# Optimization experiments

Measured on AMD Instinct MI355X. Metric: run time of the kernel, lower is better.

## Reference

```python
import jax, jax.numpy as jnp
import numpy as np

B, N, F, T = 16, 1024, 32, 12
K, FC, FT, TS, D = 3, 64, 64, 1, 16
THETA_THR = 0.6
LN_EPS = 1e-5


def setup_inputs() -> dict:
    key = jax.random.key(0)
    ks = jax.random.split(key, 20)
    r = lambda i, shape, s=0.1: jax.random.normal(ks[i], shape, dtype=jnp.float32) * s
    return dict(
        x=jax.random.normal(ks[0], (B, N, F, T), dtype=jnp.float32),
        node_embeddings=r(1, (N, D), 1.0),
        W1=r(2, (T,)), W2=r(3, (F, T)), W3=r(4, (F,)),
        bs=r(5, (1, N, N)), Vs=r(6, (N, N)),
        U1=r(7, (N,)), U2=r(8, (F, N)), U3=r(9, (F,)),
        be=r(10, (1, T, T)), Ve=r(11, (T, T)),
        Theta=r(12, (K, F, FC)),
        tc_v=r(13, (FT, FC, 1, 3)), tc_g=jnp.ones((FT,), jnp.float32), tc_b=r(14, (FT,)),
        rc_w=r(15, (FT, F, 1, 1)), rc_b=r(16, (FT,)),
        ln_w=jnp.ones((FT,), jnp.float32), ln_b=jnp.zeros((FT,), jnp.float32),
    )


def _forward(x, node_embeddings, W1, W2, W3, bs, Vs, U1, U2, U3, be, Ve,
             Theta, tc_v, tc_g, tc_b, rc_w, rc_b, ln_w, ln_b):
    b, n, f, t = x.shape
    k_order = Theta.shape[0]

    # --- temporal attention: E (B,T,T) ---
    lhs = jnp.einsum('bnft,n->btf', x, U1) @ U2                # (B,T,N)
    rhs = jnp.einsum('f,bnft->bnt', U3, x)                     # (B,N,T)
    prod = jnp.einsum('btn,bnu->btu', lhs, rhs)                # (B,T,T)
    E = jnp.einsum('ts,bsu->btu', Ve, jax.nn.sigmoid(prod + be))
    E = jax.nn.softmax(E, axis=1)

    # x_TAt = reshape(B, N*F, T) @ E  (equivalent einsum over t)
    x_TAt = jnp.einsum('bnft,btu->bnfu', x, E)                 # (B,N,F,T)

    # --- sparse spatial attention on x_TAt: (B,N,N) ---
    l2 = jnp.einsum('bnft,t->bnf', x_TAt, W1) @ W2             # (B,N,T)
    r2 = jnp.einsum('f,bnft->btn', W3, x_TAt)                  # (B,T,N)
    prod2 = jnp.einsum('bnt,btm->bnm', l2, r2)                 # (B,N,N)
    S = jnp.einsum('nm,bmk->bnk', Vs, jax.nn.sigmoid(prod2 + bs))
    Sn = jax.nn.softmax(S, axis=1)
    thr = jnp.mean(Sn) / THETA_THR
    spat = jnp.where(Sn < thr, jnp.zeros_like(Sn), Sn)         # Sparse_S_normalized

    # --- K-order adaptive graph conv with attention mask ---
    sup = jax.nn.softmax(jax.nn.relu(node_embeddings @ node_embeddings.T), axis=1)
    polys = [jnp.eye(n, dtype=x.dtype), sup]
    for k in range(2, k_order):
        polys.append(2.0 * sup @ polys[-1] - polys[-2])
    out = jnp.zeros((b, t, n, Theta.shape[2]), x.dtype)
    for k in range(k_order):
        A = polys[k][None] * spat                              # (B,N,N)
        h = jnp.einsum('bnm,bnft->btmf', A, x)                 # A^T @ x per timestep
        out = out + jnp.einsum('btmf,fo->btmo', h, Theta[k])
    gcn = jax.nn.relu(out)                                     # (B,T,N,FC)

    # --- time conv (weight-normed 1x3) + residual 1x1 conv ---
    vnorm = jnp.sqrt(jnp.sum(tc_v * tc_v, axis=(1, 2, 3), keepdims=True))
    w = tc_g[:, None, None, None] * tc_v / vnorm
    inp = gcn.transpose(0, 3, 2, 1)                            # (B,FC,N,T)
    tco = jax.lax.conv_general_dilated(
        inp, w, (1, TS), ((0, 0), (1, 1)),
        dimension_numbers=('NCHW', 'OIHW', 'NCHW')) + tc_b[None, :, None, None]
    res = jax.lax.conv_general_dilated(
        x.transpose(0, 2, 1, 3), rc_w, (1, TS), ((0, 0), (0, 0)),
        dimension_numbers=('NCHW', 'OIHW', 'NCHW')) + rc_b[None, :, None, None]

    # --- layernorm over channel dim ---
    y = (res + tco).transpose(0, 3, 2, 1)                      # (B,T,N,FT)
    mu = jnp.mean(y, axis=-1, keepdims=True)
    var = jnp.var(y, axis=-1, keepdims=True)
    y = (y - mu) / jnp.sqrt(var + LN_EPS) * ln_w + ln_b
    x_res = y.transpose(0, 2, 3, 1)                            # (B,N,FT,T)
    return x_res, spat


def reference(x, node_embeddings, W1, W2, W3, bs, Vs, U1, U2, U3, be, Ve,
              Theta, tc_v, tc_g, tc_b, rc_w, rc_b, ln_w, ln_b):
    return _forward(x, node_embeddings, W1, W2, W3, bs, Vs, U1, U2, U3, be, Ve,
                    Theta, tc_v, tc_g, tc_b, rc_w, rc_b, ln_w, ln_b)
```

## Files before the change

kernel.cpp:

```cpp
#include <hip/hip_runtime.h>
#include <math.h>

#define NB 16
#define NN 1024
#define NF 32
#define NT 12
#define NFC 64
#define NFT 64

typedef __attribute__((ext_vector_type(8))) short bf16x8;
typedef __attribute__((ext_vector_type(4))) float f32x4;

__device__ inline unsigned short cvt_bf(float f) {
    unsigned int u = __float_as_uint(f);
    u += 0x7fff + ((u >> 16) & 1);
    return (unsigned short)(u >> 16);
}
__device__ inline float bf2f(unsigned short u) {
    return __uint_as_float(((unsigned int)u) << 16);
}
__device__ inline void gll16(const short* g, short* l) {
    __builtin_amdgcn_global_load_lds((const __attribute__((address_space(1))) void*)g,
                                     (__attribute__((address_space(3))) void*)l, 16, 0, 0);
}

__global__ __launch_bounds__(384) void k_pre(const float* __restrict__ x,
                                             const float* __restrict__ U1,
                                             const float* __restrict__ U3,
                                             const float* __restrict__ W3,
                                             float* __restrict__ lhs_pre,
                                             float* __restrict__ rhs,
                                             float* __restrict__ rr3,
                                             unsigned short* __restrict__ Xrow)
{
    __shared__ float xs[8 * 384];
    int b = blockIdx.x, ch = blockIdx.y, tid = threadIdx.x;
    float acc = 0.f;
    for (int c8 = 0; c8 < 8; c8++) {
        int n0 = ch * 64 + c8 * 8;
        size_t r0 = (size_t)b * NN + n0;
        __syncthreads();
        for (int i = 0; i < 8; i++) xs[i * 384 + tid] = x[(r0 + i) * 384 + tid];
        __syncthreads();
        for (int i = 0; i < 8; i++) acc += xs[i * 384 + tid] * U1[n0 + i];
        for (int idx = tid; idx < 1536; idx += 384) {
            int row = idx / 192, jj = (idx - row * 192) * 2;
            unsigned int w = (unsigned int)cvt_bf(xs[row * 384 + jj])
                           | ((unsigned int)cvt_bf(xs[row * 384 + jj + 1]) << 16);
            *(unsigned int*)(Xrow + (r0 + row) * 384 + jj) = w;
        }
        if (tid < 192) {
            int half = tid / 96;
            int r = tid - half * 96;
            int i = r / 12, t = r - i * 12;
            const float* wv = half ? W3 : U3;
            float s = 0.f;
            for (int f = 0; f < 32; f++) s += wv[f] * xs[i * 384 + f * 12 + t];
            float* outp = half ? rr3 : rhs;
            outp[(r0 + i) * 12 + t] = s;
        }
    }
    int f = tid / 12, t = tid - f * 12;
    atomicAdd(&lhs_pre[b * 384 + t * 32 + f], acc);
}

__global__ __launch_bounds__(256) void k_lhs(const float* __restrict__ lhs_pre,
                                             const float* __restrict__ U2,
                                             float* __restrict__ lhs)
{
    int bt = blockIdx.x;
    int tid = threadIdx.x;
    __shared__ float lp[32];
    if (tid < 32) lp[tid] = lhs_pre[bt * 32 + tid];
    __syncthreads();
    for (int q = 0; q < 4; q++) {
        int n = q * 256 + tid;
        float a = 0.f;
        for (int f = 0; f < 32; f++) a += lp[f] * U2[f * NN + n];
        lhs[(size_t)bt * NN + n] = a;
    }
}

__global__ __launch_bounds__(64) void k_prod(const float* __restrict__ lhs,
                                             const float* __restrict__ rhs,
                                             float* __restrict__ prod)
{
    int blk = blockIdx.x;
    int b = blk / 144, r = blk - b * 144;
    int s = r / 12, u = r - s * 12;
    int tid = threadIdx.x;
    float p = 0.f;
    for (int n = tid; n < NN; n += 64)
        p += lhs[((size_t)b * 12 + s) * NN + n] * rhs[((size_t)b * NN + n) * 12 + u];
    for (int o = 32; o > 0; o >>= 1) p += __shfl_xor(p, o);
    if (tid == 0) prod[blk] = p;
}

__global__ __launch_bounds__(192) void k_E(const float* __restrict__ prod,
                                           const float* __restrict__ be,
                                           const float* __restrict__ Ve,
                                           const float* __restrict__ W1,
                                           float* __restrict__ E,
                                           float* __restrict__ EW1)
{
    int b = blockIdx.x, tid = threadIdx.x;
    __shared__ float ssig[144], sE[144], mx[12], sm[12];
    if (tid < 144) ssig[tid] = 1.f / (1.f + expf(-(prod[b * 144 + tid] + be[tid])));
    __syncthreads();
    if (tid < 144) {
        int t = tid / 12, u = tid - t * 12;
        float a = 0.f;
        for (int s2 = 0; s2 < 12; s2++) a += Ve[t * 12 + s2] * ssig[s2 * 12 + u];
        sE[tid] = a;
    }
    __syncthreads();
    if (tid < 12) {
        float m = -1e30f;
        for (int t = 0; t < 12; t++) m = fmaxf(m, sE[t * 12 + tid]);
        float s = 0.f;
        for (int t = 0; t < 12; t++) s += expf(sE[t * 12 + tid] - m);
        mx[tid] = m; sm[tid] = s;
    }
    __syncthreads();
    float val = 0.f;
    if (tid < 144) {
        int u = tid % 12;
        val = expf(sE[tid] - mx[u]) / sm[u];
        E[b * 144 + tid] = val;
    }
    __syncthreads();
    if (tid < 144) sE[tid] = val;
    __syncthreads();
    if (tid < 12) {
        float a = 0.f;
        for (int u = 0; u < 12; u++) a += sE[tid * 12 + u] * W1[u];
        EW1[b * 12 + tid] = a;
    }
}

__global__ __launch_bounds__(384) void k_l2r2x(const unsigned short* __restrict__ Xrow,
                                               const float* __restrict__ rr3,
                                               const float* __restrict__ E,
                                               const float* __restrict__ EW1,
                                               const float* __restrict__ W2,
                                               float* __restrict__ l2,
                                               float* __restrict__ r2)
{
    __shared__ float xs[8 * 384];
    __shared__ float Es[144], ew[12], rrs[96], lp[8][32];
    int b = blockIdx.y, tid = threadIdx.x;
    int n0 = blockIdx.x * 8;
    size_t r0 = (size_t)b * NN + n0;
    if (tid < 144) Es[tid] = E[b * 144 + tid];
    if (tid < 12) ew[tid] = EW1[b * 12 + tid];
    if (tid < 96) rrs[tid] = rr3[(r0 + tid / 12) * 12 + (tid % 12)];
    const unsigned int* Xr = (const unsigned int*)(Xrow + r0 * 384);
    for (int i2 = tid; i2 < 1536; i2 += 384) {
        unsigned int w = Xr[i2];
        xs[2 * i2]     = bf2f((unsigned short)(w & 0xffff));
        xs[2 * i2 + 1] = bf2f((unsigned short)(w >> 16));
    }
    __syncthreads();
    if (tid < 256) {
        int i = tid >> 5, f = tid & 31;
        float a = 0.f;
#pragma unroll
        for (int t = 0; t < 12; t++) a += xs[i * 384 + f * 12 + t] * ew[t];
        lp[i][f] = a;
    }
    __syncthreads();
    if (tid < 96) {
        int i = tid / 12, u = tid - i * 12;
        float a = 0.f;
        for (int f = 0; f < 32; f++) a += lp[i][f] * W2[f * 12 + u];
        l2[(r0 + i) * 12 + u] = a;
        float rv = 0.f;
#pragma unroll
        for (int t = 0; t < 12; t++) rv += rrs[i * 12 + t] * Es[t * 12 + u];
        r2[((size_t)b * 12 + u) * NN + n0 + i] = rv;
    }
}

__global__ __launch_bounds__(256) void k_xt(const unsigned short* __restrict__ Xrow,
                                            unsigned short* __restrict__ Xt)
{
    __shared__ unsigned short tl[64][66];
    int b = blockIdx.z;
    int n0 = blockIdx.y * 64, j0 = blockIdx.x * 64;
    int tid = threadIdx.x;
    int c = tid & 63, r0 = tid >> 6;
    for (int i = 0; i < 16; i++) {
        int r = r0 + i * 4;
        tl[r][c] = Xrow[((size_t)b * NN + n0 + r) * 384 + j0 + c];
    }
    __syncthreads();
    int c2 = tid & 31, r4 = tid >> 5;
    unsigned short* ob = Xt + ((size_t)b * 384 + j0) * NN + n0;
    for (int i = 0; i < 8; i++) {
        int jr = r4 + i * 8;
        unsigned int v0 = (unsigned int)tl[2 * c2][jr] | ((unsigned int)tl[2 * c2 + 1][jr] << 16);
        *(unsigned int*)(ob + (size_t)jr * NN + 2 * c2) = v0;
    }
}

__global__ __launch_bounds__(256) void k_Ptile(const float* __restrict__ l2,
                                               const float* __restrict__ r2,
                                               const float* __restrict__ bsin,
                                               unsigned short* __restrict__ Pt)
{
    __shared__ float l2s[64][13];
    __shared__ float r2s[12][64];
    __shared__ float bsS[64][65];
    int k0 = blockIdx.x * 64, m0 = blockIdx.y * 64, b = blockIdx.z;
    int tid = threadIdx.x;
    for (int i = tid; i < 768; i += 256) {
        int r = i / 12, t = i - r * 12;
        l2s[r][t] = l2[((size_t)b * NN + m0 + r) * 12 + t];
    }
    for (int i = tid; i < 768; i += 256) {
        int t = i >> 6, k = i & 63;
        r2s[t][k] = r2[((size_t)b * 12 + t) * NN + k0 + k];
    }
    for (int i = tid; i < 4096; i += 256) {
        int r = i >> 6, c = i & 63;
        bsS[r][c] = bsin[(size_t)(m0 + r) * NN + k0 + c];
    }
    __syncthreads();
    int m = tid & 63, kg = tid >> 6;
    float lv[12];
#pragma unroll
    for (int t = 0; t < 12; t++) lv[t] = l2s[m][t];
#pragma unroll
    for (int s = 0; s < 16; s++) {
        int kl = kg * 16 + s;
        float p = bsS[m][kl];
#pragma unroll
        for (int t = 0; t < 12; t++) p += lv[t] * r2s[t][kl];
        float sg = 1.f / (1.f + expf(-p));
        Pt[((size_t)b * NN + k0 + kl) * NN + m0 + m] = cvt_bf(sg);
    }
}

__global__ __launch_bounds__(256) void k_cvt(const float* __restrict__ s,
                                             unsigned short* __restrict__ d)
{
    size_t i = ((size_t)blockIdx.x * 256 + threadIdx.x) * 4;
    float4 v = *(const float4*)(s + i);
    unsigned int p0 = (unsigned int)cvt_bf(v.x) | ((unsigned int)cvt_bf(v.y) << 16);
    unsigned int p1 = (unsigned int)cvt_bf(v.z) | ((unsigned int)cvt_bf(v.w) << 16);
    *(unsigned int*)(d + i) = p0;
    *(unsigned int*)(d + i + 2) = p1;
}

__global__ __launch_bounds__(256) void k_tb16(const unsigned short* __restrict__ s,
                                              unsigned short* __restrict__ d)
{
    __shared__ unsigned short tl[64][65];
    int r0 = blockIdx.y * 64, c0 = blockIdx.x * 64;
    int tid = threadIdx.x;
    int c = tid & 63, rr = tid >> 6;
    for (int i = 0; i < 16; i++)
        tl[rr + i * 4][c] = s[(size_t)(r0 + rr + i * 4) * NN + c0 + c];
    __syncthreads();
    for (int i = 0; i < 16; i++)
        d[(size_t)(c0 + rr + i * 4) * NN + r0 + c] = tl[c][rr + i * 4];
}

__device__ inline void stage2(const short* __restrict__ g, int grow0, int gk0,
                              short* dstbase, int tid)
{
#pragma unroll
    for (int o = 0; o < 2; o++) {
        int y = o * 8192 + tid * 16;
        int rowh = y >> 7;
        int colb = (y & 127) ^ ((rowh & 7) << 4);
        const short* src = g + (size_t)(grow0 + rowh) * NN + gk0 + (colb >> 1);
        gll16(src, dstbase + (y >> 1));
    }
}

__global__ __launch_bounds__(512, 2) void sgemm8(const short* __restrict__ A,
                                                 const short* __restrict__ Bm,
                                                 float* __restrict__ C,
                                                 float* __restrict__ colsum)
{
    int bz = blockIdx.z;
    const short* Bb = Bm + (size_t)bz * NN * NN;
    int i0 = blockIdx.y * 256, j0 = blockIdx.x * 256;
    __shared__ short sm[65536];
    int tid = threadIdx.x;
    int ln = tid & 63, wv = tid >> 6;
    int wm = (wv >> 2) * 128, wn = (wv & 3) * 64;
    int fr = ln & 15, fk = ln >> 4;
    int ahalf = wv >> 2;
    int bhalf = wn >> 7;
    int bcol = wn & 64;
    int swz = (fr & 7) << 4;
    int kcol0 = ((fk * 16) ^ swz) >> 1;
    int kcol1 = ((64 + fk * 16) ^ swz) >> 1;

    f32x4 acc[8][4];
#pragma unroll
    for (int m = 0; m < 8; m++)
#pragma unroll
        for (int n = 0; n < 4; n++) acc[m][n] = (f32x4)(0.f);

    stage2(Bb, j0 + 0,   0,  sm + 16384,        tid);
    stage2(Bb, j0 + 128, 0,  sm + 16384 + 8192, tid);
    stage2(A,  i0 + 0,   0,  sm + 0,            tid);
    stage2(A,  i0 + 128, 0,  sm + 8192,         tid);
    stage2(Bb, j0 + 0,   64, sm + 32768 + 16384,        tid);
    stage2(Bb, j0 + 128, 64, sm + 32768 + 16384 + 8192, tid);
    asm volatile("s_waitcnt vmcnt(4)" ::: "memory");
    __builtin_amdgcn_s_barrier();

    for (int i = 0; i < 8; i++) {
        bf16x8 bv[8];
#pragma unroll
        for (int ph = 0; ph < 8; ph++) {
            int t = 2 * i + (ph >> 2);
            int p = t & 1;
            int q = ph & 3;
            int abase = p * 32768 + ahalf * 8192;
            int bbase = p * 32768 + 16384 + bhalf * 8192;
            if (q == 0) {
#pragma unroll
                for (int nj = 0; nj < 4; nj++) {
                    int browh = bcol + nj * 16 + fr;
                    bv[nj * 2 + 0] = *(const bf16x8*)(sm + bbase + browh * 64 + kcol0);
                    bv[nj * 2 + 1] = *(const bf16x8*)(sm + bbase + browh * 64 + kcol1);
                }
            }
            bf16x8 av[4];
#pragma unroll
            for (int m2 = 0; m2 < 2; m2++) {
                int rowh = (2 * q + m2) * 16 + fr;
                av[m2 * 2 + 0] = *(const bf16x8*)(sm + abase + rowh * 64 + kcol0);
                av[m2 * 2 + 1] = *(const bf16x8*)(sm + abase + rowh * 64 + kcol1);
            }
            {
                int st, smat, shalf;
                if (ph == 0)      { st = 2 * i + 1; smat = 0; shalf = 0; }
                else if (ph == 1) { st = 2 * i + 1; smat = 0; shalf = 1; }
                else if (ph == 2) { st = 2 * i + 2; smat = 1; shalf = 0; }
                else if (ph == 3) { st = 2 * i + 2; smat = 1; shalf = 1; }
                else if (ph == 4) { st = 2 * i + 2; smat = 0; shalf = 0; }
                else if (ph == 5) { st = 2 * i + 2; smat = 0; shalf = 1; }
                else if (ph == 6) { st = 2 * i + 3; smat = 1; shalf = 0; }
                else              { st = 2 * i + 3; smat = 1; shalf = 1; }
                if (st < 16) {
                    short* dst = sm + (st & 1) * 32768 + smat * 16384 + shalf * 8192;
                    const short* g = smat ? Bb : A;
                    int grow0 = (smat ? j0 : i0) + shalf * 128;
                    stage2(g, grow0, st * 64, dst, tid);
                }
            }
            __builtin_amdgcn_s_barrier();
            __builtin_amdgcn_s_setprio(1);
#pragma unroll
            for (int m2 = 0; m2 < 2; m2++)
#pragma unroll
                for (int nj = 0; nj < 4; nj++) {
                    acc[2 * q + m2][nj] = __builtin_amdgcn_mfma_f32_16x16x32_bf16(
                        av[m2 * 2 + 0], bv[nj * 2 + 0], acc[2 * q + m2][nj], 0, 0, 0);
                    acc[2 * q + m2][nj] = __builtin_amdgcn_mfma_f32_16x16x32_bf16(
                        av[m2 * 2 + 1], bv[nj * 2 + 1], acc[2 * q + m2][nj], 0, 0, 0);
                }
            __builtin_amdgcn_s_setprio(0);
            if (ph == 3 || ph == 7) {
                if (i < 7) asm volatile("s_waitcnt vmcnt(4)" ::: "memory");
                else       asm volatile("s_waitcnt vmcnt(0)" ::: "memory");
            }
            __builtin_amdgcn_s_barrier();
        }
    }
    float* Cb = C + (size_t)bz * NN * NN;
#pragma unroll
    for (int nj = 0; nj < 4; nj++) {
        int col = j0 + wn + nj * 16 + fr;
        float cs = 0.f;
#pragma unroll
        for (int m = 0; m < 8; m++) {
            int row = i0 + wm + m * 16 + fk * 4;
#pragma unroll
            for (int r = 0; r < 4; r++) {
                float e = expf(acc[m][nj][r]);
                Cb[(size_t)(row + r) * NN + col] = e;
                cs += e;
            }
        }
        cs += __shfl_xor(cs, 16);
        cs += __shfl_xor(cs, 32);
        if (ln < 16) atomicAdd(&colsum[(size_t)bz * NN + col], cs);
    }
}

template<int MODE>
__global__ __launch_bounds__(256) void mgemm(const short* __restrict__ A,
                                             const short* __restrict__ B,
                                             void* __restrict__ Cv,
                                             int Kd, int kchunk,
                                             int ldA, int ldB, int ldC,
                                             long sA, long sB, long sC,
                                             float* __restrict__ colsum)
{
    int bz = blockIdx.z;
    const short* Ab = A + (size_t)bz * sA;
    const short* Bb = B + (size_t)bz * sB;
    int i0 = blockIdx.y * 128, j0 = blockIdx.x * 128;
    __shared__ short sm[16384];
    int tid = threadIdx.x;
    int ln = tid & 63, wv = tid >> 6;
    int wm = (wv >> 1) * 64, wn = (wv & 1) * 64;
    int fr = ln & 15, fk = ln >> 4;
    f32x4 acc[4][4];
#pragma unroll
    for (int a = 0; a < 4; a++)
#pragma unroll
        for (int b2 = 0; b2 < 4; b2++) acc[a][b2] = (f32x4)(0.f);

    int k_lo = 0, k_hi = Kd;
    if constexpr (MODE == 3) { k_lo = bz * kchunk; k_hi = k_lo + kchunk; }

    for (int k0 = k_lo; k0 < k_hi; k0 += 64) {
#pragma unroll
        for (int q = 0; q < 4; q++) {
            int e = q * 2048 + tid * 8;
            const short* src = Ab + (size_t)(i0 + (e >> 6)) * ldA + k0 + (e & 63);
            gll16(src, sm + e);
        }
#pragma unroll
        for (int q = 0; q < 4; q++) {
            int e = q * 2048 + tid * 8;
            const short* src = Bb + (size_t)(j0 + (e >> 6)) * ldB + k0 + (e & 63);
            gll16(src, sm + 8192 + e);
        }
        __syncthreads();
#pragma unroll
        for (int ks = 0; ks < 2; ks++) {
            bf16x8 av[4], bv[4];
#pragma unroll
            for (int mi = 0; mi < 4; mi++)
                av[mi] = *(const bf16x8*)(sm + (wm + mi * 16 + fr) * 64 + ks * 32 + fk * 8);
#pragma unroll
            for (int nj = 0; nj < 4; nj++)
                bv[nj] = *(const bf16x8*)(sm + 8192 + (wn + nj * 16 + fr) * 64 + ks * 32 + fk * 8);
#pragma unroll
            for (int mi = 0; mi < 4; mi++)
#pragma unroll
                for (int nj = 0; nj < 4; nj++)
                    acc[mi][nj] = __builtin_amdgcn_mfma_f32_16x16x32_bf16(av[mi], bv[nj], acc[mi][nj], 0, 0, 0);
        }
        __syncthreads();
    }
    if constexpr (MODE == 3) {
        float* Cb = (float*)Cv;
#pragma unroll
        for (int mi = 0; mi < 4; mi++)
#pragma unroll
            for (int nj = 0; nj < 4; nj++) {
                int row = i0 + wm + mi * 16 + fk * 4;
                int col = j0 + wn + nj * 16 + fr;
#pragma unroll
                for (int r = 0; r < 4; r++)
                    atomicAdd(&Cb[(size_t)(row + r) * ldC + col], acc[mi][nj][r]);
            }
    }
}

__global__ __launch_bounds__(256) void mgemm_h(const short* __restrict__ A,
                                               const short* __restrict__ B,
                                               unsigned short* __restrict__ C)
{
    int id = blockIdx.x;
    int xcd = id & 7, jj = id >> 3;
    int b = (xcd << 1) | (jj / 24);
    int r = jj % 24;
    int i0 = (r / 3) * 128, j0 = (r % 3) * 128;
    const short* Ab = A + (size_t)b * NN * NN;
    const short* Bb = B + (size_t)b * 384 * NN;
    __shared__ short sm[16384];
    int tid = threadIdx.x;
    int ln = tid & 63, wv = tid >> 6;
    int wm = (wv >> 1) * 64, wn = (wv & 1) * 64;
    int fr = ln & 15, fk = ln >> 4;
    f32x4 acc[4][4];
#pragma unroll
    for (int a = 0; a < 4; a++)
#pragma unroll
        for (int b2 = 0; b2 < 4; b2++) acc[a][b2] = (f32x4)(0.f);

    for (int k0 = 0; k0 < NN; k0 += 64) {
#pragma unroll
        for (int q = 0; q < 4; q++) {
            int e = q * 2048 + tid * 8;
            gll16(Ab + (size_t)(i0 + (e >> 6)) * NN + k0 + (e & 63), sm + e);
        }
#pragma unroll
        for (int q = 0; q < 4; q++) {
            int e = q * 2048 + tid * 8;
            gll16(Bb + (size_t)(j0 + (e >> 6)) * NN + k0 + (e & 63), sm + 8192 + e);
        }
        __syncthreads();
#pragma unroll
        for (int ks = 0; ks < 2; ks++) {
            bf16x8 av[4], bv[4];
#pragma unroll
            for (int mi = 0; mi < 4; mi++)
                av[mi] = *(const bf16x8*)(sm + (wm + mi * 16 + fr) * 64 + ks * 32 + fk * 8);
#pragma unroll
            for (int nj = 0; nj < 4; nj++)
                bv[nj] = *(const bf16x8*)(sm + 8192 + (wn + nj * 16 + fr) * 64 + ks * 32 + fk * 8);
#pragma unroll
            for (int mi = 0; mi < 4; mi++)
#pragma unroll
                for (int nj = 0; nj < 4; nj++)
                    acc[mi][nj] = __builtin_amdgcn_mfma_f32_16x16x32_bf16(av[mi], bv[nj], acc[mi][nj], 0, 0, 0);
        }
        __syncthreads();
    }
#pragma unroll
    for (int mi = 0; mi < 4; mi++)
#pragma unroll
        for (int nj = 0; nj < 4; nj++) {
            int row = i0 + wm + mi * 16 + fk * 4;
            int col = j0 + wn + nj * 16 + fr;
#pragma unroll
            for (int r2 = 0; r2 < 4; r2++)
                C[((size_t)b * NN + row + r2) * 384 + col] = cvt_bf(acc[mi][nj][r2]);
        }
}

__global__ __launch_bounds__(256) void k_normprep2(float* __restrict__ spat,
                                                   const float* __restrict__ colsum,
                                                   const float* __restrict__ sup,
                                                   const float* __restrict__ supsq,
                                                   unsigned short* __restrict__ At1,
                                                   unsigned short* __restrict__ At2,
                                                   float* __restrict__ sdiag)
{
    __shared__ unsigned short t1[64][66];
    __shared__ unsigned short t2[64][66];
    int b = blockIdx.z;
    int n0 = blockIdx.y * 64, m0 = blockIdx.x * 64;
    int tid = threadIdx.x;
    int c = tid & 63, r0 = tid >> 6;
    const float thr = (1.0f / 1024.0f) / 0.6f;
    float inv = 1.f / colsum[(size_t)b * NN + m0 + c];
    float* sp = spat + (size_t)b * NN * NN;
    for (int i = 0; i < 16; i++) {
        int r = r0 + i * 4;
        size_t idx = (size_t)(n0 + r) * NN + m0 + c;
        float v = sp[idx] * inv;
        v = (v < thr) ? 0.f : v;
        sp[idx] = v;
        if (n0 + r == m0 + c) sdiag[(size_t)b * NN + n0 + r] = v;
        t1[r][c] = cvt_bf(sup[(size_t)(n0 + r) * NN + m0 + c] * v);
        float p2 = 2.f * supsq[(size_t)(n0 + r) * NN + m0 + c]
                 - (((n0 + r) == (m0 + c)) ? 1.f : 0.f);
        t2[r][c] = cvt_bf(p2 * v);
    }
    __syncthreads();
    int c2 = tid & 31, r4 = tid >> 5;
    size_t ob = ((size_t)b * NN + m0) * NN + n0;
    for (int i = 0; i < 8; i++) {
        int rr = r4 + i * 8;
        unsigned int v1 = (unsigned int)t1[2 * c2][rr] | ((unsigned int)t1[2 * c2 + 1][rr] << 16);
        unsigned int v2 = (unsigned int)t2[2 * c2][rr] | ((unsigned int)t2[2 * c2 + 1][rr] << 16);
        *(unsigned int*)(At1 + ob + (size_t)rr * NN + 2 * c2) = v1;
        *(unsigned int*)(At2 + ob + (size_t)rr * NN + 2 * c2) = v2;
    }
}

__global__ __launch_bounds__(256) void k_sup(const float* __restrict__ emb,
                                             float* __restrict__ sup,
                                             unsigned short* __restrict__ supB)
{
    int n = blockIdx.x, tid = threadIdx.x;
    __shared__ float en[16];
    if (tid < 16) en[tid] = emb[n * 16 + tid];
    __syncthreads();
    float v[4];
#pragma unroll
    for (int q = 0; q < 4; q++) {
        int m = q * 256 + tid;
        float d = 0.f;
#pragma unroll
        for (int dd = 0; dd < 16; dd++) d += en[dd] * emb[m * 16 + dd];
        v[q] = fmaxf(d, 0.f);
    }
    float mx = fmaxf(fmaxf(v[0], v[1]), fmaxf(v[2], v[3]));
    for (int o = 32; o > 0; o >>= 1) mx = fmaxf(mx, __shfl_xor(mx, o));
    __shared__ float red[4];
    if ((tid & 63) == 0) red[tid >> 6] = mx;
    __syncthreads();
    mx = fmaxf(fmaxf(red[0], red[1]), fmaxf(red[2], red[3]));
    float e[4];
    float s = 0.f;
#pragma unroll
    for (int q = 0; q < 4; q++) { e[q] = expf(v[q] - mx); s += e[q]; }
    for (int o = 32; o > 0; o >>= 1) s += __shfl_xor(s, o);
    __shared__ float red2[4];
    if ((tid & 63) == 0) red2[tid >> 6] = s;
    __syncthreads();
    s = red2[0] + red2[1] + red2[2] + red2[3];
    float inv = 1.f / s;
#pragma unroll
    for (int q = 0; q < 4; q++) {
        float val = e[q] * inv;
        sup[(size_t)n * NN + q * 256 + tid] = val;
        supB[(size_t)n * NN + q * 256 + tid] = cvt_bf(val);
    }
}

__global__ __launch_bounds__(256) void k_wprep(const float* __restrict__ tcv,
                                               const float* __restrict__ tcg,
                                               const float* __restrict__ Theta,
                                               const float* __restrict__ rcw,
                                               unsigned short* __restrict__ Wr,
                                               unsigned short* __restrict__ Th,
                                               unsigned short* __restrict__ Rc)
{
    int tid = threadIdx.x;
    if (blockIdx.x < 64) {
        int o = blockIdx.x;
        float t = 0.f, p = 0.f;
        if (tid < 192) { t = tcv[o * 192 + tid]; p = t * t; }
        for (int off = 32; off > 0; off >>= 1) p += __shfl_xor(p, off);
        __shared__ float wsr[3];
        if (tid < 192 && (tid & 63) == 0) wsr[tid >> 6] = p;
        __syncthreads();
        if (tid < 192) {
            float sum = wsr[0] + wsr[1] + wsr[2];
            int c = tid / 3, dt = tid - c * 3;
            Wr[o * 192 + dt * 64 + c] = cvt_bf(t * (tcg[o] / sqrtf(sum)));
        }
    } else {
        for (int i = tid; i < 6144; i += 256) {
            int o = i / 96, rem = i - o * 96;
            int kind = rem >> 5, f = rem & 31;
            Th[i] = cvt_bf(Theta[kind * 2048 + f * 64 + o]);
        }
        for (int i = tid; i < 2048; i += 256) Rc[i] = cvt_bf(rcw[i]);
    }
}

__global__ __launch_bounds__(256) void k_tail(const float* __restrict__ x,
                                              const unsigned short* __restrict__ h1,
                                              const unsigned short* __restrict__ h2,
                                              const float* __restrict__ sdiag,
                                              const unsigned short* __restrict__ Th,
                                              const unsigned short* __restrict__ Wr,
                                              const unsigned short* __restrict__ Rc,
                                              const float* __restrict__ tcb,
                                              const float* __restrict__ rcb,
                                              const float* __restrict__ lnw,
                                              const float* __restrict__ lnb,
                                              float* __restrict__ out)
{
    int b = blockIdx.y;
    int node0 = blockIdx.x * 4;
    int tid = threadIdx.x;
    int ln = tid & 63, wv = tid >> 6;
    int fr = ln & 15, fk = ln >> 4;

    __shared__ union {
        struct { unsigned short xt[1920], h1t[1920], h2t[1920], gcn[4032]; } a;
        float Y[48 * 65];
    } u;
    __shared__ float sdp[48];
    __shared__ float lnwS[64], lnbS[64], tbS[64];
    __shared__ float muS[48], rsS[48];

    size_t rowb = ((size_t)b * NN + node0) * 384;
    {
        const float2* xp = (const float2*)(x + rowb);
        const unsigned int* h1p = (const unsigned int*)(h1 + rowb);
        const unsigned int* h2p = (const unsigned int*)(h2 + rowb);
        for (int q = tid; q < 768; q += 256) {
            int j0 = q * 2;
            int node = j0 / 384, j = j0 - node * 384;
            int f = j / 12, t = j - f * 12;
            int t2 = t + 1, f2 = f;
            if (t2 == 12) { t2 = 0; f2 = f + 1; }
            int la0 = node * 480 + t * 40 + f;
            int la1 = node * 480 + t2 * 40 + f2;
            float2 xv = xp[q];
            unsigned int w1 = h1p[q], w2 = h2p[q];
            u.a.xt[la0] = cvt_bf(xv.x);  u.a.xt[la1] = cvt_bf(xv.y);
            u.a.h1t[la0] = (unsigned short)(w1 & 0xffff); u.a.h1t[la1] = (unsigned short)(w1 >> 16);
            u.a.h2t[la0] = (unsigned short)(w2 & 0xffff); u.a.h2t[la1] = (unsigned short)(w2 >> 16);
        }
    }
    for (int i = tid; i < 576; i += 256) {
        int node = i / 144, r = i - node * 144;
        int rr = (r < 72) ? 0 : 13;
        u.a.gcn[node * 1008 + rr * 72 + (r % 72)] = 0;
    }
    if (tid < 48) sdp[tid] = sdiag[(size_t)b * NN + node0 + tid / 12];
    if (tid < 64) { lnwS[tid] = lnw[tid]; lnbS[tid] = lnb[tid]; tbS[tid] = tcb[tid] + rcb[tid]; }

    int ocol = wv * 16 + fr;
    bf16x8 bTh[3], bWr[6], bRc;
#pragma unroll
    for (int kb = 0; kb < 3; kb++)
        bTh[kb] = *(const bf16x8*)((const short*)Th + (size_t)ocol * 96 + kb * 32 + fk * 8);
#pragma unroll
    for (int kb = 0; kb < 6; kb++)
        bWr[kb] = *(const bf16x8*)((const short*)Wr + (size_t)ocol * 192 + kb * 32 + fk * 8);
    bRc = *(const bf16x8*)((const short*)Rc + (size_t)ocol * 32 + fk * 8);

    int na[3], ta[3];
#pragma unroll
    for (int rb = 0; rb < 3; rb++) {
        int p = rb * 16 + fr;
        na[rb] = p / 12; ta[rb] = p - na[rb] * 12;
    }
    __syncthreads();

    f32x4 acc[3];
#pragma unroll
    for (int rb = 0; rb < 3; rb++) {
        int ax = na[rb] * 480 + ta[rb] * 40 + fk * 8;
        bf16x8 avx = *(const bf16x8*)(u.a.xt + ax);
        f32x4 z = (f32x4)(0.f);
        acc[rb] = __builtin_amdgcn_mfma_f32_16x16x32_bf16(avx, bTh[0], z, 0, 0, 0);
#pragma unroll
        for (int r = 0; r < 4; r++) acc[rb][r] *= sdp[rb * 16 + fk * 4 + r];
        bf16x8 av1 = *(const bf16x8*)(u.a.h1t + ax);
        acc[rb] = __builtin_amdgcn_mfma_f32_16x16x32_bf16(av1, bTh[1], acc[rb], 0, 0, 0);
        bf16x8 av2 = *(const bf16x8*)(u.a.h2t + ax);
        acc[rb] = __builtin_amdgcn_mfma_f32_16x16x32_bf16(av2, bTh[2], acc[rb], 0, 0, 0);
    }
#pragma unroll
    for (int rb = 0; rb < 3; rb++) {
#pragma unroll
        for (int r = 0; r < 4; r++) {
            int pc = rb * 16 + fk * 4 + r;
            int nc = pc / 12, tc2 = pc - nc * 12;
            u.a.gcn[nc * 1008 + (tc2 + 1) * 72 + wv * 16 + fr] = cvt_bf(fmaxf(acc[rb][r], 0.f));
        }
    }
    __syncthreads();
#pragma unroll
    for (int rb = 0; rb < 3; rb++) {
        f32x4 a2 = (f32x4)(0.f);
#pragma unroll
        for (int kb = 0; kb < 6; kb++) {
            int dt = kb >> 1, c0 = (kb & 1) * 32;
            bf16x8 ag = *(const bf16x8*)(u.a.gcn + na[rb] * 1008 + (ta[rb] + dt) * 72 + c0 + fk * 8);
            a2 = __builtin_amdgcn_mfma_f32_16x16x32_bf16(ag, bWr[kb], a2, 0, 0, 0);
        }
        int ax = na[rb] * 480 + ta[rb] * 40 + fk * 8;
        bf16x8 avx = *(const bf16x8*)(u.a.xt + ax);
        acc[rb] = __builtin_amdgcn_mfma_f32_16x16x32_bf16(avx, bRc, a2, 0, 0, 0);
    }
    __syncthreads();
    float tb = tbS[ocol];
#pragma unroll
    for (int rb = 0; rb < 3; rb++)
#pragma unroll
        for (int r = 0; r < 4; r++)
            u.Y[(rb * 16 + fk * 4 + r) * 65 + ocol] = acc[rb][r] + tb;
    __syncthreads();
    if (tid < 48) {
        float s = 0.f, s2 = 0.f;
        for (int o = 0; o < 64; o++) {
            float v = u.Y[tid * 65 + o];
            s += v; s2 += v * v;
        }
        float mm = s * (1.f / 64.f);
        float var = s2 * (1.f / 64.f) - mm * mm;
        muS[tid] = mm; rsS[tid] = rsqrtf(var + 1e-5f);
    }
    __syncthreads();
    float2* obv = (float2*)(out + rowb * 2);
    for (int q = tid; q < 1536; q += 256) {
        int i = q * 2;
        int node = i / 768, rr = i - node * 768;
        int o = rr / 12, t = rr - o * 12;
        int p0 = node * 12 + t;
        float v0 = (u.Y[p0 * 65 + o] - muS[p0]) * rsS[p0] * lnwS[o] + lnbS[o];
        int t1 = t + 1, o1 = o;
        if (t1 == 12) { t1 = 0; o1 = o + 1; }
        int p1 = node * 12 + t1;
        float v1 = (u.Y[p1 * 65 + o1] - muS[p1]) * rsS[p1] * lnwS[o1] + lnbS[o1];
        float2 pk; pk.x = v0; pk.y = v1;
        obv[q] = pk;
    }
}

extern "C" void kernel_launch(void* const* d_in, const int* in_sizes, int n_in,
                              void* d_out, int out_size, void* d_ws, size_t ws_size,
                              hipStream_t stream)
{
    const float* x    = (const float*)d_in[0];
    const float* emb  = (const float*)d_in[1];
    const float* W1   = (const float*)d_in[2];
    const float* W2   = (const float*)d_in[3];
    const float* W3   = (const float*)d_in[4];
    const float* bs   = (const float*)d_in[5];
    const float* Vs   = (const float*)d_in[6];
    const float* U1   = (const float*)d_in[7];
    const float* U2   = (const float*)d_in[8];
    const float* U3   = (const float*)d_in[9];
    const float* be   = (const float*)d_in[10];
    const float* Ve   = (const float*)d_in[11];
    const float* Theta= (const float*)d_in[12];
    const float* tcv  = (const float*)d_in[13];
    const float* tcg  = (const float*)d_in[14];
    const float* tcb  = (const float*)d_in[15];
    const float* rcw  = (const float*)d_in[16];
    const float* rcb  = (const float*)d_in[17];
    const float* lnw  = (const float*)d_in[18];
    const float* lnb  = (const float*)d_in[19];

    float* xres = (float*)d_out;
    float* spat = xres + (size_t)NB * NN * NFT * NT;

    char* base = (char*)d_ws;
    unsigned short* Xrow = (unsigned short*)(base + 0);
    unsigned short* Pt   = (unsigned short*)(base + 0);
    unsigned short* supB = (unsigned short*)(base + 0);
    unsigned short* supT = (unsigned short*)(base + 2097152);
    unsigned short* At1  = (unsigned short*)(base + 0);
    unsigned short* At2  = (unsigned short*)xres;
    unsigned short* Xt  = (unsigned short*)(base + 33554432);
    unsigned short* h1  = (unsigned short*)(base + 46137344);
    unsigned short* h2  = (unsigned short*)(base + 58720256);
    unsigned short* Vsb = (unsigned short*)(base + 71303168);
    float* colsum  = (float*)(base + 73400320);
    float* sdiag   = (float*)(base + 73465856);
    float* sup     = (float*)(base + 77594624);
    float* supsq   = (float*)(base + 81788928);
    float* lhs_pre = (float*)(base + 85983232);
    float* lhs     = (float*)(base + 86007808);
    float* rhs     = (float*)(base + 86794240);
    float* rr3     = (float*)(base + 87580672);
    float* prod    = (float*)(base + 88367104);
    float* E       = (float*)(base + 88376320);
    float* EW1     = (float*)(base + 88385536);
    float* l2      = (float*)(base + 88386560);
    float* r2      = (float*)(base + 89172992);
    unsigned short* Wr = (unsigned short*)(base + 89959424);
    unsigned short* Th = (unsigned short*)(base + 89984000);
    unsigned short* Rc = (unsigned short*)(base + 89996288);

    hipMemsetAsync(lhs_pre, 0, 6144 * sizeof(float), stream);
    hipMemsetAsync(supsq, 0, (size_t)NN * NN * sizeof(float), stream);

    k_pre<<<dim3(16, 16), 384, 0, stream>>>(x, U1, U3, W3, lhs_pre, rhs, rr3, Xrow);
    k_lhs<<<192, 256, 0, stream>>>(lhs_pre, U2, lhs);
    k_prod<<<2304, 64, 0, stream>>>(lhs, rhs, prod);
    k_E<<<16, 192, 0, stream>>>(prod, be, Ve, W1, E, EW1);
    k_l2r2x<<<dim3(128, 16), 384, 0, stream>>>(Xrow, rr3, E, EW1, W2, l2, r2);
    k_xt<<<dim3(6, 16, 16), 256, 0, stream>>>(Xrow, Xt);
    k_Ptile<<<dim3(16, 16, 16), 256, 0, stream>>>(l2, r2, bs, Pt);
    k_cvt<<<1024, 256, 0, stream>>>(Vs, Vsb);
    hipMemsetAsync(colsum, 0, (size_t)NB * NN * sizeof(float), stream);
    sgemm8<<<dim3(4, 4, 16), 512, 0, stream>>>((const short*)Vsb, (const short*)Pt,
                                               spat, colsum);
    k_sup<<<1024, 256, 0, stream>>>(emb, sup, supB);
    k_tb16<<<dim3(16, 16), 256, 0, stream>>>(supB, supT);
    mgemm<3><<<dim3(8, 8, 4), 256, 0, stream>>>((const short*)supB, (const short*)supT,
        (void*)supsq, NN, 256, NN, NN, NN, 0L, 0L, 0L, nullptr);
    k_normprep2<<<dim3(16, 16, 16), 256, 0, stream>>>(spat, colsum, sup, supsq, At1, At2, sdiag);
    mgemm_h<<<384, 256, 0, stream>>>((const short*)At1, (const short*)Xt, h1);
    mgemm_h<<<384, 256, 0, stream>>>((const short*)At2, (const short*)Xt, h2);
    k_wprep<<<65, 256, 0, stream>>>(tcv, tcg, Theta, rcw, Wr, Th, Rc);
    k_tail<<<dim3(256, 16), 256, 0, stream>>>(x, h1, h2, sdiag, Th, Wr, Rc,
                                              tcb, rcb, lnw, lnb, xres);
}
```

Measured before the change: 316.3 us.

## Reassociate temporal-attention product, merge Vs conversion and the two h GEMMs

The temporal attention product is reassociated: instead of forming lhs (B,T,N) via U2 and then reducing over N, it computes M2 = U2·rhs (B,F,T) and contracts it with lhs_pre inside k_E, which removes two kernels and the large lhs intermediate. The Vs-to-bf16 conversion is folded into the k_xt transpose kernel, and the two mgemm_h launches are merged into a single 768-block launch. These changes aim to cut launch overhead and memory traffic. In exchange they add atomics in k_M2, change the floating-point summation order, and require zeroing the larger memset region that now covers M2.

```diff
diff --git a/kernel.cpp b/kernel.cpp
--- a/kernel.cpp
+++ b/kernel.cpp
@@ -64,39 +64,21 @@
     atomicAdd(&lhs_pre[b * 384 + t * 32 + f], acc);
 }
 
-__global__ __launch_bounds__(256) void k_lhs(const float* __restrict__ lhs_pre,
-                                             const float* __restrict__ U2,
-                                             float* __restrict__ lhs)
-{
-    int bt = blockIdx.x;
-    int tid = threadIdx.x;
-    __shared__ float lp[32];
-    if (tid < 32) lp[tid] = lhs_pre[bt * 32 + tid];
-    __syncthreads();
-    for (int q = 0; q < 4; q++) {
-        int n = q * 256 + tid;
-        float a = 0.f;
-        for (int f = 0; f < 32; f++) a += lp[f] * U2[f * NN + n];
-        lhs[(size_t)bt * NN + n] = a;
-    }
-}
-
-__global__ __launch_bounds__(64) void k_prod(const float* __restrict__ lhs,
-                                             const float* __restrict__ rhs,
-                                             float* __restrict__ prod)
-{
-    int blk = blockIdx.x;
-    int b = blk / 144, r = blk - b * 144;
-    int s = r / 12, u = r - s * 12;
-    int tid = threadIdx.x;
-    float p = 0.f;
-    for (int n = tid; n < NN; n += 64)
-        p += lhs[((size_t)b * 12 + s) * NN + n] * rhs[((size_t)b * NN + n) * 12 + u];
-    for (int o = 32; o > 0; o >>= 1) p += __shfl_xor(p, o);
-    if (tid == 0) prod[blk] = p;
-}
-
-__global__ __launch_bounds__(192) void k_E(const float* __restrict__ prod,
+__global__ __launch_bounds__(384) void k_M2(const float* __restrict__ U2,
+                                            const float* __restrict__ rhs,
+                                            float* __restrict__ M2)
+{
+    int b = blockIdx.x, ch = blockIdx.y, tid = threadIdx.x;
+    int f = tid / 12, u = tid - (tid / 12) * 12;
+    int n0 = ch * 32;
+    float a = 0.f;
+    for (int n = n0; n < n0 + 32; n++)
+        a += U2[(size_t)f * NN + n] * rhs[((size_t)b * NN + n) * 12 + u];
+    atomicAdd(&M2[b * 384 + f * 12 + u], a);
+}
+
+__global__ __launch_bounds__(192) void k_E(const float* __restrict__ lhs_pre,
+                                           const float* __restrict__ M2,
                                            const float* __restrict__ be,
                                            const float* __restrict__ Ve,
                                            const float* __restrict__ W1,
@@ -104,8 +86,20 @@
                                            float* __restrict__ EW1)
 {
     int b = blockIdx.x, tid = threadIdx.x;
+    __shared__ float lp2[384], m2s[384];
     __shared__ float ssig[144], sE[144], mx[12], sm[12];
-    if (tid < 144) ssig[tid] = 1.f / (1.f + expf(-(prod[b * 144 + tid] + be[tid])));
+    for (int i = tid; i < 384; i += 192) {
+        lp2[i] = lhs_pre[b * 384 + i];
+        m2s[i] = M2[b * 384 + i];
+    }
+    __syncthreads();
+    if (tid < 144) {
+        int s = tid / 12, u = tid - s * 12;
+        float p = 0.f;
+#pragma unroll
+        for (int f = 0; f < 32; f++) p += lp2[s * 32 + f] * m2s[f * 12 + u];
+        ssig[tid] = 1.f / (1.f + expf(-(p + be[tid])));
+    }
     __syncthreads();
     if (tid < 144) {
         int t = tid / 12, u = tid - t * 12;
@@ -182,12 +176,23 @@
 }
 
 __global__ __launch_bounds__(256) void k_xt(const unsigned short* __restrict__ Xrow,
-                                            unsigned short* __restrict__ Xt)
-{
+                                            unsigned short* __restrict__ Xt,
+                                            const float* __restrict__ Vs,
+                                            unsigned short* __restrict__ Vsb)
+{
+    int tid = threadIdx.x;
+    int fid = blockIdx.x + 6 * (blockIdx.y + 16 * blockIdx.z);
+    if (fid < 1024) {
+        size_t i = (size_t)fid * 1024 + tid * 4;
+        float4 v = *(const float4*)(Vs + i);
+        unsigned int p0 = (unsigned int)cvt_bf(v.x) | ((unsigned int)cvt_bf(v.y) << 16);
+        unsigned int p1 = (unsigned int)cvt_bf(v.z) | ((unsigned int)cvt_bf(v.w) << 16);
+        *(unsigned int*)(Vsb + i) = p0;
+        *(unsigned int*)(Vsb + i + 2) = p1;
+    }
     __shared__ unsigned short tl[64][66];
     int b = blockIdx.z;
     int n0 = blockIdx.y * 64, j0 = blockIdx.x * 64;
-    int tid = threadIdx.x;
     int c = tid & 63, r0 = tid >> 6;
     for (int i = 0; i < 16; i++) {
         int r = r0 + i * 4;
@@ -239,17 +244,6 @@
         float sg = 1.f / (1.f + expf(-p));
         Pt[((size_t)b * NN + k0 + kl) * NN + m0 + m] = cvt_bf(sg);
     }
-}
-
-__global__ __launch_bounds__(256) void k_cvt(const float* __restrict__ s,
-                                             unsigned short* __restrict__ d)
-{
-    size_t i = ((size_t)blockIdx.x * 256 + threadIdx.x) * 4;
-    float4 v = *(const float4*)(s + i);
-    unsigned int p0 = (unsigned int)cvt_bf(v.x) | ((unsigned int)cvt_bf(v.y) << 16);
-    unsigned int p1 = (unsigned int)cvt_bf(v.z) | ((unsigned int)cvt_bf(v.w) << 16);
-    *(unsigned int*)(d + i) = p0;
-    *(unsigned int*)(d + i + 2) = p1;
 }
 
 __global__ __launch_bounds__(256) void k_tb16(const unsigned short* __restrict__ s,
@@ -468,17 +462,22 @@
     }
 }
 
-__global__ __launch_bounds__(256) void mgemm_h(const short* __restrict__ A,
-                                               const short* __restrict__ B,
-                                               unsigned short* __restrict__ C)
+__global__ __launch_bounds__(256) void mgemm_hh(const short* __restrict__ A1,
+                                                const short* __restrict__ A2,
+                                                const short* __restrict__ B,
+                                                unsigned short* __restrict__ C1,
+                                                unsigned short* __restrict__ C2)
 {
     int id = blockIdx.x;
-    int xcd = id & 7, jj = id >> 3;
+    int half = id / 384;
+    int sid = id - half * 384;
+    int xcd = sid & 7, jj = sid >> 3;
     int b = (xcd << 1) | (jj / 24);
     int r = jj % 24;
     int i0 = (r / 3) * 128, j0 = (r % 3) * 128;
-    const short* Ab = A + (size_t)b * NN * NN;
+    const short* Ab = (half ? A2 : A1) + (size_t)b * NN * NN;
     const short* Bb = B + (size_t)b * 384 * NN;
+    unsigned short* C = half ? C2 : C1;
     __shared__ short sm[16384];
     int tid = threadIdx.x;
     int ln = tid & 63, wv = tid >> 6;
@@ -834,10 +833,9 @@
     float* sup     = (float*)(base + 77594624);
     float* supsq   = (float*)(base + 81788928);
     float* lhs_pre = (float*)(base + 85983232);
-    float* lhs     = (float*)(base + 86007808);
+    float* M2      = (float*)(base + 86007808);
     float* rhs     = (float*)(base + 86794240);
     float* rr3     = (float*)(base + 87580672);
-    float* prod    = (float*)(base + 88367104);
     float* E       = (float*)(base + 88376320);
     float* EW1     = (float*)(base + 88385536);
     float* l2      = (float*)(base + 88386560);
@@ -846,17 +844,15 @@
     unsigned short* Th = (unsigned short*)(base + 89984000);
     unsigned short* Rc = (unsigned short*)(base + 89996288);
 
-    hipMemsetAsync(lhs_pre, 0, 6144 * sizeof(float), stream);
+    hipMemsetAsync(lhs_pre, 0, 49152, stream);
     hipMemsetAsync(supsq, 0, (size_t)NN * NN * sizeof(float), stream);
 
     k_pre<<<dim3(16, 16), 384, 0, stream>>>(x, U1, U3, W3, lhs_pre, rhs, rr3, Xrow);
-    k_lhs<<<192, 256, 0, stream>>>(lhs_pre, U2, lhs);
-    k_prod<<<2304, 64, 0, stream>>>(lhs, rhs, prod);
-    k_E<<<16, 192, 0, stream>>>(prod, be, Ve, W1, E, EW1);
+    k_M2<<<dim3(16, 32), 384, 0, stream>>>(U2, rhs, M2);
+    k_E<<<16, 192, 0, stream>>>(lhs_pre, M2, be, Ve, W1, E, EW1);
     k_l2r2x<<<dim3(128, 16), 384, 0, stream>>>(Xrow, rr3, E, EW1, W2, l2, r2);
-    k_xt<<<dim3(6, 16, 16), 256, 0, stream>>>(Xrow, Xt);
+    k_xt<<<dim3(6, 16, 16), 256, 0, stream>>>(Xrow, Xt, Vs, Vsb);
     k_Ptile<<<dim3(16, 16, 16), 256, 0, stream>>>(l2, r2, bs, Pt);
-    k_cvt<<<1024, 256, 0, stream>>>(Vs, Vsb);
     hipMemsetAsync(colsum, 0, (size_t)NB * NN * sizeof(float), stream);
     sgemm8<<<dim3(4, 4, 16), 512, 0, stream>>>((const short*)Vsb, (const short*)Pt,
                                                spat, colsum);
@@ -865,8 +861,8 @@
     mgemm<3><<<dim3(8, 8, 4), 256, 0, stream>>>((const short*)supB, (const short*)supT,
         (void*)supsq, NN, 256, NN, NN, NN, 0L, 0L, 0L, nullptr);
     k_normprep2<<<dim3(16, 16, 16), 256, 0, stream>>>(spat, colsum, sup, supsq, At1, At2, sdiag);
-    mgemm_h<<<384, 256, 0, stream>>>((const short*)At1, (const short*)Xt, h1);
-    mgemm_h<<<384, 256, 0, stream>>>((const short*)At2, (const short*)Xt, h2);
+    mgemm_hh<<<768, 256, 0, stream>>>((const short*)At1, (const short*)At2,
+                                      (const short*)Xt, h1, h2);
     k_wprep<<<65, 256, 0, stream>>>(tcv, tcg, Theta, rcw, Wr, Th, Rc);
     k_tail<<<dim3(256, 16), 256, 0, stream>>>(x, h1, h2, sdiag, Th, Wr, Rc,
                                               tcb, rcb, lnw, lnb, xres);
```

New measurement: 290.4 us. -8.2%, faster.
